# Kernel optimization log

Hardware: AMD Instinct MI355X
Metric: run time of the kernel (lower is better)

## Reference

```python
import jax, jax.numpy as jnp
import numpy as np

D_MODEL = 1024
NUM_HEADS = 16
HEAD_DIM = D_MODEL // NUM_HEADS


def setup_inputs() -> dict:
    key = jax.random.key(0)
    ks = jax.random.split(key, 5)
    x = jax.random.normal(ks[0], (2, 2048, D_MODEL), dtype=jnp.float32)
    # torch nn.Linear init scale ~ U(-1/sqrt(in), 1/sqrt(in)); use small normals
    s = 1.0 / np.sqrt(D_MODEL)
    W_qkv = jax.random.normal(ks[1], (D_MODEL, 3 * D_MODEL), dtype=jnp.float32) * s
    b_qkv = jax.random.normal(ks[2], (3 * D_MODEL,), dtype=jnp.float32) * s
    W_out = jax.random.normal(ks[3], (D_MODEL, D_MODEL), dtype=jnp.float32) * s
    b_out = jax.random.normal(ks[4], (D_MODEL,), dtype=jnp.float32) * s
    return {"x": x, "W_qkv": W_qkv, "b_qkv": b_qkv, "W_out": W_out, "b_out": b_out}


def reference(x, W_qkv, b_qkv, W_out, b_out):
    B, S, _ = x.shape
    qkv = x @ W_qkv + b_qkv                                  # [B,S,3D]
    qkv = qkv.reshape(B, S, NUM_HEADS, 3 * HEAD_DIM).transpose(0, 2, 1, 3)  # [B,H,S,3d]
    q, k, v = jnp.split(qkv, 3, axis=-1)                     # each [B,H,S,d]
    scale = 1.0 / np.sqrt(HEAD_DIM)
    scores = jnp.einsum("bhqd,bhkd->bhqk", q, k) * scale      # [B,H,S,S]
    attn = jax.nn.softmax(scores, axis=-1)
    values = jnp.einsum("bhqk,bhkd->bhqd", attn, v)           # [B,H,S,d]
    values = values.transpose(0, 2, 1, 3).reshape(B, S, D_MODEL)
    return values @ W_out + b_out
```

## Files before the change

kernel.cpp:

```cpp
#include <hip/hip_runtime.h>


#define D_MODEL 1024
#define NHEAD   16
#define HDIM    64
#define SEQ     2048
#define BATCH   2
#define NTOK    (BATCH * SEQ)

typedef float    f32x4  __attribute__((ext_vector_type(4)));
typedef float    f32x16 __attribute__((ext_vector_type(16)));
typedef _Float16 f16x8  __attribute__((ext_vector_type(8)));
typedef _Float16 f16x4  __attribute__((ext_vector_type(4)));

#define GLOBAL_LOAD_LDS16(gptr, lptr)                                            \
    __builtin_amdgcn_global_load_lds(                                            \
        (const __attribute__((address_space(1))) unsigned int*)(gptr),           \
        (__attribute__((address_space(3))) unsigned int*)(lptr), 16, 0, 0)

__global__ __launch_bounds__(256) void prep_kernel(
    const float* __restrict__ x, _Float16* __restrict__ xh,
    const float* __restrict__ Wqkv, _Float16* __restrict__ wq_t,
    const float* __restrict__ Wout, _Float16* __restrict__ wo_t)
{
    const int bx = blockIdx.x;
    const int tid = threadIdx.x;
    if (bx < 4096) {
        const int i = (bx * 256 + tid) * 4;
        const float4 v = *(const float4*)&x[i];
        f16x4 hh;
        hh[0] = (_Float16)v.x; hh[1] = (_Float16)v.y;
        hh[2] = (_Float16)v.z; hh[3] = (_Float16)v.w;
        *(f16x4*)&xh[i] = hh;
        return;
    }
    __shared__ float ts[64][65];
    const float* W; _Float16* Wt; int N, n0, k0;
    if (bx < 4096 + 768) {
        const int local = bx - 4096;
        W = Wqkv; Wt = wq_t; N = 3072;
        n0 = (local % 48) * 64; k0 = (local / 48) * 64;
    } else {
        const int local = bx - 4864;
        W = Wout; Wt = wo_t; N = 1024;
        n0 = (local % 16) * 64; k0 = (local / 16) * 64;
    }
    {
        const int r = tid >> 2, c = (tid & 3) << 4;
        const float* src = W + (size_t)(k0 + r) * N + n0 + c;
        #pragma unroll
        for (int u = 0; u < 4; ++u)
            *(float4*)&ts[r][c + u * 4] = *(const float4*)&src[u * 4];
    }
    __syncthreads();
    {
        const int n = tid >> 2, kg = (tid & 3) << 4;
        f16x8 v0, v1;
        #pragma unroll
        for (int j = 0; j < 8; ++j) {
            v0[j] = (_Float16)ts[kg + j][n];
            v1[j] = (_Float16)ts[kg + 8 + j][n];
        }
        _Float16* dst = Wt + (size_t)(n0 + n) * D_MODEL + k0 + kg;
        *(f16x8*)&dst[0] = v0;
        *(f16x8*)&dst[8] = v1;
    }
}

__global__ __launch_bounds__(512) void gemm_qkv_kernel(
    const _Float16* __restrict__ A, const _Float16* __restrict__ Bt,
    const float* __restrict__ bias, _Float16* __restrict__ Cout,
    int M, int N, int K)
{
    __shared__ _Float16 lds[2][2][4096];
    const int tid = threadIdx.x;
    const int wave = tid >> 6, lane = tid & 63;
    const int quad = lane >> 4, l16 = lane & 15;
    const int m0 = blockIdx.y * 128, n0 = blockIdx.x * 128;
    const int wr = wave >> 1, wc = wave & 1;

    f32x4 acc[2][4] = {};

    const bool isA = wave < 4;
    const _Float16* gsrc = isA ? (A + (size_t)m0 * K) : (Bt + (size_t)n0 * K);
    const int plane = isA ? 0 : 1;
    const int sbase = (wave & 3) * 2;

    #pragma unroll
    for (int j = 0; j < 2; ++j) {
        const int seg = sbase + j;
        const int chunk = seg >> 1;
        const int row = ((seg & 1) << 6) | lane;
        GLOBAL_LOAD_LDS16(gsrc + (size_t)row * K + chunk * 8, &lds[0][plane][seg * 512]);
    }
    __syncthreads();

    const int nk = K / 32;
    for (int t = 0; t < nk; ++t) {
        const int cur = t & 1;

        if (t + 1 < nk) {
            const int k1 = (t + 1) * 32;
            #pragma unroll
            for (int j = 0; j < 2; ++j) {
                const int seg = sbase + j;
                const int chunk = seg >> 1;
                const int row = ((seg & 1) << 6) | lane;
                GLOBAL_LOAD_LDS16(gsrc + (size_t)row * K + k1 + chunk * 8,
                                  &lds[cur ^ 1][plane][seg * 512]);
            }
        }

        f16x8 a[2], b[4];
        #pragma unroll
        for (int mt = 0; mt < 2; ++mt)
            a[mt] = *(const f16x8*)&lds[cur][0][quad * 1024 + (wr * 32 + mt * 16 + l16) * 8];
        #pragma unroll
        for (int nt = 0; nt < 4; ++nt)
            b[nt] = *(const f16x8*)&lds[cur][1][quad * 1024 + (wc * 64 + nt * 16 + l16) * 8];
        #pragma unroll
        for (int mt = 0; mt < 2; ++mt)
            #pragma unroll
            for (int nt = 0; nt < 4; ++nt)
                acc[mt][nt] = __builtin_amdgcn_mfma_f32_16x16x32_f16(a[mt], b[nt], acc[mt][nt], 0, 0, 0);

        __syncthreads();
    }

    #pragma unroll
    for (int nt = 0; nt < 4; ++nt) {
        const int col = n0 + wc * 64 + nt * 16 + l16;
        const float bv = bias[col];
        #pragma unroll
        for (int mt = 0; mt < 2; ++mt) {
            #pragma unroll
            for (int r = 0; r < 4; ++r) {
                const int row = m0 + wr * 32 + mt * 16 + quad * 4 + r;
                Cout[(size_t)row * N + col] = (_Float16)(acc[mt][nt][r] + bv);
            }
        }
    }
}

__global__ __launch_bounds__(512) void gemm_out_kernel(
    const _Float16* __restrict__ A, const _Float16* __restrict__ Bt,
    const float* __restrict__ bias, float* __restrict__ Cout)
{
    const int K = D_MODEL, N = D_MODEL;
    __shared__ _Float16 ldsA[2][4096];
    __shared__ _Float16 ldsB[2][2048];
    const int tid = threadIdx.x;
    const int wave = tid >> 6, lane = tid & 63;
    const int quad = lane >> 4, l16 = lane & 15;
    const int m0 = blockIdx.y * 128, n0 = blockIdx.x * 64;
    const int wr = wave >> 1, wc = wave & 1;

    f32x4 acc[2][2] = {};

    if (wave < 4) {
        #pragma unroll
        for (int j = 0; j < 2; ++j) {
            const int seg = wave * 2 + j;
            const int chunk = seg >> 1;
            const int row = ((seg & 1) << 6) | lane;
            GLOBAL_LOAD_LDS16(A + (size_t)(m0 + row) * K + chunk * 8, &ldsA[0][seg * 512]);
        }
    } else {
        const int seg = wave - 4;
        GLOBAL_LOAD_LDS16(Bt + (size_t)(n0 + lane) * K + seg * 8, &ldsB[0][seg * 512]);
    }
    __syncthreads();

    const int nk = K / 32;
    for (int t = 0; t < nk; ++t) {
        const int cur = t & 1;

        if (t + 1 < nk) {
            const int k1 = (t + 1) * 32;
            if (wave < 4) {
                #pragma unroll
                for (int j = 0; j < 2; ++j) {
                    const int seg = wave * 2 + j;
                    const int chunk = seg >> 1;
                    const int row = ((seg & 1) << 6) | lane;
                    GLOBAL_LOAD_LDS16(A + (size_t)(m0 + row) * K + k1 + chunk * 8,
                                      &ldsA[cur ^ 1][seg * 512]);
                }
            } else {
                const int seg = wave - 4;
                GLOBAL_LOAD_LDS16(Bt + (size_t)(n0 + lane) * K + k1 + seg * 8,
                                  &ldsB[cur ^ 1][seg * 512]);
            }
        }

        f16x8 a[2], b[2];
        #pragma unroll
        for (int mt = 0; mt < 2; ++mt)
            a[mt] = *(const f16x8*)&ldsA[cur][quad * 1024 + (wr * 32 + mt * 16 + l16) * 8];
        #pragma unroll
        for (int nt = 0; nt < 2; ++nt)
            b[nt] = *(const f16x8*)&ldsB[cur][quad * 512 + (wc * 32 + nt * 16 + l16) * 8];
        #pragma unroll
        for (int mt = 0; mt < 2; ++mt)
            #pragma unroll
            for (int nt = 0; nt < 2; ++nt)
                acc[mt][nt] = __builtin_amdgcn_mfma_f32_16x16x32_f16(a[mt], b[nt], acc[mt][nt], 0, 0, 0);

        __syncthreads();
    }

    #pragma unroll
    for (int nt = 0; nt < 2; ++nt) {
        const int col = n0 + wc * 32 + nt * 16 + l16;
        const float bv = bias[col];
        #pragma unroll
        for (int mt = 0; mt < 2; ++mt) {
            #pragma unroll
            for (int r = 0; r < 4; ++r) {
                const int row = m0 + wr * 32 + mt * 16 + quad * 4 + r;
                Cout[(size_t)row * N + col] = acc[mt][nt][r] + bv;
            }
        }
    }
}

__global__ __launch_bounds__(256) void swizzle_kv_kernel(
    const _Float16* __restrict__ qkv,
    _Float16* __restrict__ Ksw, _Float16* __restrict__ Vsw)
{
    __shared__ _Float16 ts[64][72];
    const int tid = threadIdx.x;
    const int s0 = blockIdx.x * 64, h = blockIdx.y, b = blockIdx.z;
    const size_t hsz = (size_t)8 * SEQ * 8;
    _Float16* kh = Ksw + (size_t)(b * NHEAD + h) * hsz;
    _Float16* vh = Vsw + (size_t)(b * NHEAD + h) * hsz;

    {
        const int s = s0 + (tid >> 2);
        const int dg = (tid & 3) << 4;
        const _Float16* src = qkv + (size_t)(b * SEQ + s) * (3 * D_MODEL) + h * (3 * HDIM) + HDIM + dg;
        const f16x8 v0 = *(const f16x8*)&src[0];
        const f16x8 v1 = *(const f16x8*)&src[8];
        const int c0 = dg >> 3;
        *(f16x8*)&kh[((size_t)c0 * SEQ + s) * 8]       = v0;
        *(f16x8*)&kh[((size_t)(c0 + 1) * SEQ + s) * 8] = v1;
    }
    {
        const int s = tid >> 2, dg = (tid & 3) << 4;
        const _Float16* src = qkv + (size_t)(b * SEQ + s0 + s) * (3 * D_MODEL) + h * (3 * HDIM) + 2 * HDIM + dg;
        *(f16x8*)&ts[s][dg]     = *(const f16x8*)&src[0];
        *(f16x8*)&ts[s][dg + 8] = *(const f16x8*)&src[8];
    }
    __syncthreads();
    {
        const int d = tid >> 2, sg = (tid & 3) << 4;
        f16x8 v0, v1;
        #pragma unroll
        for (int j = 0; j < 8; ++j) { v0[j] = ts[sg + j][d]; v1[j] = ts[sg + 8 + j][d]; }
        const int cs0 = (s0 + sg) >> 3;
        *(f16x8*)&vh[((size_t)cs0 * HDIM + d) * 8]       = v0;
        *(f16x8*)&vh[((size_t)(cs0 + 1) * HDIM + d) * 8] = v1;
    }
}

__device__ __forceinline__ void softmax_frag(
    const f32x16 s0, const f32x16 s1, float& rs, f16x8 pa[4])
{
    #pragma unroll
    for (int half = 0; half < 2; ++half) {
        const f32x16 sv = half ? s1 : s0;
        float p[16];
        #pragma unroll
        for (int r = 0; r < 16; ++r)
            p[r] = __builtin_amdgcn_exp2f(sv[r]);
        #pragma unroll
        for (int r = 0; r < 16; r += 4)
            rs += (p[r] + p[r + 1]) + (p[r + 2] + p[r + 3]);

        union { f16x8 hv; unsigned u[4]; } lo, hh;
        {
            const unsigned A = __builtin_bit_cast(unsigned, __builtin_amdgcn_cvt_pkrtz(p[0], p[1]));
            const unsigned B = __builtin_bit_cast(unsigned, __builtin_amdgcn_cvt_pkrtz(p[2], p[3]));
            const unsigned C = __builtin_bit_cast(unsigned, __builtin_amdgcn_cvt_pkrtz(p[4], p[5]));
            const unsigned D = __builtin_bit_cast(unsigned, __builtin_amdgcn_cvt_pkrtz(p[6], p[7]));
            const auto rac = __builtin_amdgcn_permlane32_swap(A, C, false, false);
            const auto rbd = __builtin_amdgcn_permlane32_swap(B, D, false, false);
            lo.u[0] = rac[0]; lo.u[1] = rbd[0]; lo.u[2] = rac[1]; lo.u[3] = rbd[1];
        }
        {
            const unsigned E = __builtin_bit_cast(unsigned, __builtin_amdgcn_cvt_pkrtz(p[8],  p[9]));
            const unsigned F = __builtin_bit_cast(unsigned, __builtin_amdgcn_cvt_pkrtz(p[10], p[11]));
            const unsigned G = __builtin_bit_cast(unsigned, __builtin_amdgcn_cvt_pkrtz(p[12], p[13]));
            const unsigned H = __builtin_bit_cast(unsigned, __builtin_amdgcn_cvt_pkrtz(p[14], p[15]));
            const auto reg = __builtin_amdgcn_permlane32_swap(E, G, false, false);
            const auto rfh = __builtin_amdgcn_permlane32_swap(F, H, false, false);
            hh.u[0] = reg[0]; hh.u[1] = rfh[0]; hh.u[2] = reg[1]; hh.u[3] = rfh[1];
        }
        pa[half * 2]     = lo.hv;
        pa[half * 2 + 1] = hh.hv;
    }
}

__global__ __launch_bounds__(512) void attn_mfma_kernel(
    const _Float16* __restrict__ qkv,
    const _Float16* __restrict__ Ksw, const _Float16* __restrict__ Vsw,
    _Float16* __restrict__ val)
{
    __shared__ _Float16 Ks[2][8192];
    __shared__ _Float16 Vts[2][8192];

    const int tid = threadIdx.x;
    const int wave = tid >> 6, lane = tid & 63;
    const int l31 = lane & 31, hi = lane >> 5;

    const int id = blockIdx.x;
    const int g  = (id & 7) * 32 + (id >> 3);
    const int qt = g & 7, hb = g >> 3;
    const int h  = hb & 15, b = hb >> 4;
    const int q0 = qt * 256;

    const size_t hsz = (size_t)8 * SEQ * 8;
    const _Float16* kh = Ksw + (size_t)(b * NHEAD + h) * hsz;
    const _Float16* vh = Vsw + (size_t)(b * NHEAD + h) * hsz;

    f16x8 qf[4];
    {
        const int row = q0 + wave * 32 + l31;
        const _Float16* src = qkv + (size_t)(b * SEQ + row) * (3 * D_MODEL) + h * (3 * HDIM) + hi * 8;
        #pragma unroll
        for (int kk = 0; kk < 4; ++kk) {
            const f16x8 t = *(const f16x8*)(src + kk * 16);
            #pragma unroll
            for (int j = 0; j < 8; ++j)
                qf[kk][j] = (_Float16)((float)t[j] * 0.1803368802f);
        }
    }

    f32x16 acc0 = {};
    f32x16 acc1 = {};
    float rs = 0.f;

    const int sidx0 = wave * 2;
    #pragma unroll
    for (int j = 0; j < 2; ++j) {
        const int idx = sidx0 + j;
        const int u = idx >> 3, c = idx & 7;
        GLOBAL_LOAD_LDS16(kh + ((size_t)c * SEQ + u * 64 + lane) * 8, &Ks[0][idx * 512]);
        GLOBAL_LOAD_LDS16(vh + ((size_t)(u * 8 + c) * HDIM + lane) * 8, &Vts[0][idx * 512]);
    }
    __syncthreads();

    for (int kt = 0; kt < SEQ / 128; ++kt) {
        const int cur = kt & 1;

        if (kt + 1 < SEQ / 128) {
            #pragma unroll
            for (int j = 0; j < 2; ++j) {
                const int idx = sidx0 + j;
                const int u = idx >> 3, c = idx & 7;
                GLOBAL_LOAD_LDS16(kh + ((size_t)c * SEQ + (kt + 1) * 128 + u * 64 + lane) * 8,
                                  &Ks[cur ^ 1][idx * 512]);
                GLOBAL_LOAD_LDS16(vh + ((size_t)((kt + 1) * 16 + u * 8 + c) * HDIM + lane) * 8,
                                  &Vts[cur ^ 1][idx * 512]);
            }
        }

        #pragma unroll
        for (int u = 0; u < 2; ++u) {
            const _Float16* ksub = &Ks[cur][u * 4096];
            const _Float16* vsub = &Vts[cur][u * 4096];

            f32x16 s0 = {}, s1 = {};
            __builtin_amdgcn_s_setprio(1);
            #pragma unroll
            for (int kk = 0; kk < 4; ++kk) {
                const f16x8 k0 = *(const f16x8*)&ksub[(kk * 2 + hi) * 512 + l31 * 8];
                const f16x8 k1 = *(const f16x8*)&ksub[(kk * 2 + hi) * 512 + (32 + l31) * 8];
                s0 = __builtin_amdgcn_mfma_f32_32x32x16_f16(k0, qf[kk], s0, 0, 0, 0);
                s1 = __builtin_amdgcn_mfma_f32_32x32x16_f16(k1, qf[kk], s1, 0, 0, 0);
            }
            __builtin_amdgcn_s_setprio(0);

            f16x8 pa[4];
            softmax_frag(s0, s1, rs, pa);

            __builtin_amdgcn_s_setprio(1);
            #pragma unroll
            for (int ks = 0; ks < 4; ++ks) {
                const f16x8 v0 = *(const f16x8*)&vsub[(ks * 2 + hi) * 512 + l31 * 8];
                const f16x8 v1 = *(const f16x8*)&vsub[(ks * 2 + hi) * 512 + (32 + l31) * 8];
                acc0 = __builtin_amdgcn_mfma_f32_32x32x16_f16(pa[ks], v0, acc0, 0, 0, 0);
                acc1 = __builtin_amdgcn_mfma_f32_32x32x16_f16(pa[ks], v1, acc1, 0, 0, 0);
            }
            __builtin_amdgcn_s_setprio(0);
        }

        __syncthreads();
    }

    rs += __shfl_xor(rs, 32);
    const float inv = 1.f / rs;

    #pragma unroll
    for (int r = 0; r < 16; ++r) {
        const int qo = (r & 3) + 8 * (r >> 2) + 4 * hi;
        const float invr = __shfl(inv, qo);
        const int row = b * SEQ + q0 + wave * 32 + qo;
        val[(size_t)row * D_MODEL + h * HDIM + l31]      = (_Float16)(acc0[r] * invr);
        val[(size_t)row * D_MODEL + h * HDIM + 32 + l31] = (_Float16)(acc1[r] * invr);
    }
}

extern "C" void kernel_launch(void* const* d_in, const int* in_sizes, int n_in,
                              void* d_out, int out_size, void* d_ws, size_t ws_size,
                              hipStream_t stream)
{
    const float* x     = (const float*)d_in[0];
    const float* W_qkv = (const float*)d_in[1];
    const float* b_qkv = (const float*)d_in[2];
    const float* W_out = (const float*)d_in[3];
    const float* b_out = (const float*)d_in[4];

    char* ws = (char*)d_ws;
    _Float16* Ksw   = (_Float16*)ws;
    _Float16* val_h = (_Float16*)(ws + (8u << 20));
    _Float16* wq_t  = (_Float16*)(ws + (16u << 20));
    _Float16* wo_t  = (_Float16*)(ws + (22u << 20));
    _Float16* qkv_h = (_Float16*)(ws + (24u << 20));
    _Float16* x_h   = (_Float16*)(ws + (48u << 20));
    _Float16* Vsw   = (_Float16*)(ws + (48u << 20));

    prep_kernel<<<5120, 256, 0, stream>>>(x, x_h, W_qkv, wq_t, W_out, wo_t);
    gemm_qkv_kernel<<<dim3(3 * D_MODEL / 128, NTOK / 128), 512, 0, stream>>>(
        x_h, wq_t, b_qkv, qkv_h, NTOK, 3 * D_MODEL, D_MODEL);
    swizzle_kv_kernel<<<dim3(SEQ / 64, NHEAD, BATCH), 256, 0, stream>>>(qkv_h, Ksw, Vsw);
    attn_mfma_kernel<<<dim3(256, 1, 1), 512, 0, stream>>>(qkv_h, Ksw, Vsw, val_h);
    gemm_out_kernel<<<dim3(D_MODEL / 64, NTOK / 128), 512, 0, stream>>>(
        val_h, wo_t, b_out, (float*)d_out);
}
```

Before: 216.8 us.

## Triple-buffer QKV GEMM LDS loads with explicit vmcnt gating and MFMA priority

Changes the QKV projection GEMM from double- to triple-buffered LDS staging with a prefetch distance of two K-steps. Explicit s_waitcnt vmcnt gates and barriers replace __syncthreads, and s_setprio raises wave priority around the MFMA block. The aim is to hide more global-load latency behind compute, at the cost of more LDS per block, which may lower occupancy.

```diff
diff --git a/kernel.cpp b/kernel.cpp
--- a/kernel.cpp
+++ b/kernel.cpp
@@ -72,7 +72,7 @@
     const float* __restrict__ bias, _Float16* __restrict__ Cout,
     int M, int N, int K)
 {
-    __shared__ _Float16 lds[2][2][4096];
+    __shared__ _Float16 lds[3][2][4096];
     const int tid = threadIdx.x;
     const int wave = tid >> 6, lane = tid & 63;
     const int quad = lane >> 4, l16 = lane & 15;
@@ -86,46 +86,56 @@
     const int plane = isA ? 0 : 1;
     const int sbase = (wave & 3) * 2;
 
-    #pragma unroll
-    for (int j = 0; j < 2; ++j) {
-        const int seg = sbase + j;
-        const int chunk = seg >> 1;
-        const int row = ((seg & 1) << 6) | lane;
-        GLOBAL_LOAD_LDS16(gsrc + (size_t)row * K + chunk * 8, &lds[0][plane][seg * 512]);
-    }
-    __syncthreads();
+#define G1_STAGE(tt, bi) {                                                     \
+        const int _k1 = (tt) * 32;                                             \
+        _Pragma("unroll")                                                      \
+        for (int _j = 0; _j < 2; ++_j) {                                       \
+            const int _seg = sbase + _j;                                       \
+            const int _row = ((_seg & 1) << 6) | lane;                         \
+            GLOBAL_LOAD_LDS16(gsrc + (size_t)_row * K + _k1 + (_seg >> 1) * 8, \
+                              &lds[bi][plane][_seg * 512]);                    \
+        } }
+
+#define G1_COMPUTE(bi) {                                                       \
+        f16x8 a[2], b[4];                                                      \
+        _Pragma("unroll")                                                      \
+        for (int mt = 0; mt < 2; ++mt)                                         \
+            a[mt] = *(const f16x8*)&lds[bi][0][quad * 1024 + (wr * 32 + mt * 16 + l16) * 8]; \
+        _Pragma("unroll")                                                      \
+        for (int nt = 0; nt < 4; ++nt)                                         \
+            b[nt] = *(const f16x8*)&lds[bi][1][quad * 1024 + (wc * 64 + nt * 16 + l16) * 8]; \
+        __builtin_amdgcn_s_setprio(1);                                         \
+        _Pragma("unroll")                                                      \
+        for (int mt = 0; mt < 2; ++mt)                                         \
+            _Pragma("unroll")                                                  \
+            for (int nt = 0; nt < 4; ++nt)                                     \
+                acc[mt][nt] = __builtin_amdgcn_mfma_f32_16x16x32_f16(a[mt], b[nt], acc[mt][nt], 0, 0, 0); \
+        __builtin_amdgcn_s_setprio(0); }
+
+#define G1_KSTEP(t, gatestr) {                                                 \
+        const int _cur = (t) % 3;                                              \
+        if ((t) + 2 < nk) { G1_STAGE((t) + 2, ((t) + 2) % 3); }                \
+        asm volatile("s_waitcnt " gatestr ::: "memory");                       \
+        __builtin_amdgcn_s_barrier();                                          \
+        __builtin_amdgcn_sched_barrier(0);                                     \
+        G1_COMPUTE(_cur);                                                      \
+        __builtin_amdgcn_sched_barrier(0);                                     \
+        __builtin_amdgcn_s_barrier();                                          \
+        __builtin_amdgcn_sched_barrier(0);                                     \
+    }
 
     const int nk = K / 32;
-    for (int t = 0; t < nk; ++t) {
-        const int cur = t & 1;
-
-        if (t + 1 < nk) {
-            const int k1 = (t + 1) * 32;
-            #pragma unroll
-            for (int j = 0; j < 2; ++j) {
-                const int seg = sbase + j;
-                const int chunk = seg >> 1;
-                const int row = ((seg & 1) << 6) | lane;
-                GLOBAL_LOAD_LDS16(gsrc + (size_t)row * K + k1 + chunk * 8,
-                                  &lds[cur ^ 1][plane][seg * 512]);
-            }
-        }
-
-        f16x8 a[2], b[4];
-        #pragma unroll
-        for (int mt = 0; mt < 2; ++mt)
-            a[mt] = *(const f16x8*)&lds[cur][0][quad * 1024 + (wr * 32 + mt * 16 + l16) * 8];
-        #pragma unroll
-        for (int nt = 0; nt < 4; ++nt)
-            b[nt] = *(const f16x8*)&lds[cur][1][quad * 1024 + (wc * 64 + nt * 16 + l16) * 8];
-        #pragma unroll
-        for (int mt = 0; mt < 2; ++mt)
-            #pragma unroll
-            for (int nt = 0; nt < 4; ++nt)
-                acc[mt][nt] = __builtin_amdgcn_mfma_f32_16x16x32_f16(a[mt], b[nt], acc[mt][nt], 0, 0, 0);
-
-        __syncthreads();
-    }
+    G1_STAGE(0, 0);
+    G1_STAGE(1, 1);
+
+    for (int t = 0; t < nk - 2; ++t)
+        G1_KSTEP(t, "vmcnt(4)");
+    G1_KSTEP(nk - 2, "vmcnt(2)");
+    G1_KSTEP(nk - 1, "vmcnt(0)");
+
+#undef G1_KSTEP
+#undef G1_COMPUTE
+#undef G1_STAGE
 
     #pragma unroll
     for (int nt = 0; nt < 4; ++nt) {
```

Measured after the change: 211.5 us. 1.03x faster.
